# Performance work log

Hardware: AMD Instinct MI355X
Metric: run time of the kernel (lower is better)

Reference implementation:

```python
import jax, jax.numpy as jnp
import numpy as np

B, NSTEP, NSAMPLE = 16, 32, 10
EMBED, STATE, VOCAB, TOTAL = 128, 512, 32000, 8192
STD_SCALE = 0.113
EPS = 1e-5


def setup_inputs() -> dict:
    key = jax.random.key(0)
    ks = jax.random.split(key, 9)
    g = lambda k, shape: jax.random.normal(k, shape, jnp.float32) * 0.05
    return {
        "zi": jax.random.randint(ks[0], (B,), 0, TOTAL),
        "y": jax.random.randint(ks[1], (B, NSTEP), 0, VOCAB),
        "rd": jax.random.uniform(ks[2], (NSTEP, B, NSAMPLE), jnp.float32),
        "latent": g(ks[3], (TOTAL, EMBED)),
        "state_pref_W": g(ks[4], (STATE, 2 * EMBED)),
        "state_pref_b": g(ks[5], (STATE,)),
        "state_move": g(ks[6], (STATE, EMBED)),
        "vocab_W": g(ks[7], (VOCAB, EMBED)),
        "vocab_b": g(ks[8], (VOCAB,)),
    }


def reference(zi, y, rd, latent, state_pref_W, state_pref_b, state_move, vocab_W, vocab_b):
    # z: [B, NSAMPLE, D] -- latent row per batch element, repeated over samples
    z0 = jnp.repeat(latent[zi][:, None, :], NSAMPLE, axis=1)

    def step(carry, rd_t):
        z, zold, lp = carry
        # per-step normalization (torch std is unbiased, ddof=1)
        z = z / (EPS + jnp.std(z, axis=-1, ddof=1, keepdims=True)) * STD_SCALE
        pref = jnp.concatenate([zold, z], axis=-1) @ state_pref_W.T + state_pref_b  # [B,S,STATE]
        xp = jax.nn.softmax(pref, axis=-1)
        xpc = jnp.cumsum(xp, axis=-1)
        # first index where rd < cumulative prob (argmax of bool = first True)
        which = jnp.argmax(rd_t[:, :, None] < xpc, axis=-1)  # [B,S]
        xps = jnp.take_along_axis(xp, which[:, :, None], axis=-1)[..., 0]
        lp = lp + jnp.log(xps)
        mvs = state_move[which]  # [B,S,D]
        return (z + mvs, z, mvs), mvs

    init = (z0, jnp.zeros_like(z0), jnp.zeros((B, NSAMPLE), jnp.float32))
    # note: carry slot 2 of init is lp=0; fix tuple to match step outputs
    init = (z0, jnp.zeros_like(z0), jnp.zeros((B, NSAMPLE), jnp.float32))

    def step_fixed(carry, rd_t):
        z, zold, lp = carry
        z = z / (EPS + jnp.std(z, axis=-1, ddof=1, keepdims=True)) * STD_SCALE
        pref = jnp.concatenate([zold, z], axis=-1) @ state_pref_W.T + state_pref_b
        xp = jax.nn.softmax(pref, axis=-1)
        xpc = jnp.cumsum(xp, axis=-1)
        which = jnp.argmax(rd_t[:, :, None] < xpc, axis=-1)
        xps = jnp.take_along_axis(xp, which[:, :, None], axis=-1)[..., 0]
        lp = lp + jnp.log(xps)
        mvs = state_move[which]
        return (z + mvs, z, lp), mvs

    (_, _, lp), emits = jax.lax.scan(step_fixed, init, rd)  # emits: [T,B,S,D]
    emits = jnp.transpose(emits, (1, 0, 2, 3))  # [B,T,S,D]
    ys = jax.nn.log_softmax(emits @ vocab_W.T + vocab_b, axis=-1)  # [B,T,S,V]
    idx = jnp.broadcast_to(y[:, :, None, None], (B, NSTEP, NSAMPLE, 1))
    yp = jnp.take_along_axis(ys, idx, axis=-1)[..., 0]  # [B,T,S]
    return yp.mean(axis=2)  # [B,T]
```

## Files before the change

### kernel.cpp

```cpp
#include <hip/hip_runtime.h>
#include <hip/hip_bf16.h>

#define B_ 16
#define T_ 32
#define NS_ 10
#define D_ 128
#define ST_ 512
#define V_ 32000
#define NCHAIN 160
#define NLOGZ 250
#define NBLK2 (NCHAIN + NLOGZ)

using short8  = __attribute__((ext_vector_type(8))) short;
using f32x4   = __attribute__((ext_vector_type(4))) float;
using half8   = __attribute__((ext_vector_type(8))) _Float16;
using half2v  = __attribute__((ext_vector_type(2))) _Float16;

__device__ __forceinline__ unsigned short f2bf(float f){
  unsigned u = __float_as_uint(f);
  u += 0x7FFFu + ((u >> 16) & 1u);
  return (unsigned short)(u >> 16);
}
__device__ __forceinline__ unsigned packbf(float a, float b){
  return ((unsigned)f2bf(b) << 16) | (unsigned)f2bf(a);
}
__device__ __forceinline__ unsigned short f2h(float f){
  return __builtin_bit_cast(unsigned short, (_Float16)f);
}
__device__ __forceinline__ float h2f(unsigned u, int hi){
  half2v h = __builtin_bit_cast(half2v, u);
  return (float)h[hi];
}
__device__ __forceinline__ float readlane_f(float v, int lane){
  return __int_as_float(__builtin_amdgcn_readlane(__float_as_int(v), lane));
}

#define DPPADD(x, ctrl, rm) { \
  int _t = __builtin_amdgcn_update_dpp(0, __float_as_int(x), ctrl, rm, 0xf, true); \
  x += __int_as_float(_t); }

__global__ __launch_bounds__(256) void prep_kernel(
    const int* __restrict__ zi, const float* __restrict__ latent,
    const float* __restrict__ prefW, const float* __restrict__ move,
    unsigned short* __restrict__ Hh, unsigned short* __restrict__ Lh,
    unsigned short* __restrict__ Gh,
    float* __restrict__ HU0, float* __restrict__ LU0, float* __restrict__ D0,
    float2* __restrict__ S0, float2* __restrict__ SM,
    unsigned* __restrict__ mbf, float* __restrict__ partial,
    float* __restrict__ out, int* __restrict__ logzdone,
    int* __restrict__ scandone)
{
  const int bid = blockIdx.x, t = threadIdx.x;
  const int lane = t & 63, wv = t >> 6;
  const int c16 = lane & 15, q = lane >> 4;

  if (bid < 192){
    const int sg = bid / 24, tile = bid % 24;
    half8 afr[4][4];
    #pragma unroll
    for (int rt = 0; rt < 4; ++rt){
      const float* mp = move + (sg*64 + rt*16 + c16)*D_ + q*8;
      #pragma unroll
      for (int kk = 0; kk < 4; ++kk){
        float4 f0 = *(const float4*)(mp + kk*32);
        float4 f1 = *(const float4*)(mp + kk*32 + 4);
        half8 a;
        a[0]=(_Float16)f0.x; a[1]=(_Float16)f0.y; a[2]=(_Float16)f0.z; a[3]=(_Float16)f0.w;
        a[4]=(_Float16)f1.x; a[5]=(_Float16)f1.y; a[6]=(_Float16)f1.z; a[7]=(_Float16)f1.w;
        afr[rt][kk] = a;
      }
    }
    const int ct = tile*64 + wv*16 + c16;
    const float* bp; unsigned short* base; int ccol;
    if (ct < 512)      { bp = prefW + ct*256 + 128; base = Hh; ccol = ct; }
    else if (ct < 1024){ bp = prefW + (ct-512)*256; base = Lh; ccol = ct-512; }
    else               { bp = move + (ct-1024)*128; base = Gh; ccol = ct-1024; }
    half8 bfr[4];
    #pragma unroll
    for (int kk = 0; kk < 4; ++kk){
      float4 f0 = *(const float4*)(bp + q*8 + kk*32);
      float4 f1 = *(const float4*)(bp + q*8 + kk*32 + 4);
      half8 bb;
      bb[0]=(_Float16)f0.x; bb[1]=(_Float16)f0.y; bb[2]=(_Float16)f0.z; bb[3]=(_Float16)f0.w;
      bb[4]=(_Float16)f1.x; bb[5]=(_Float16)f1.y; bb[6]=(_Float16)f1.z; bb[7]=(_Float16)f1.w;
      bfr[kk] = bb;
    }
    #pragma unroll
    for (int rt = 0; rt < 4; ++rt){
      f32x4 acc = {0.f,0.f,0.f,0.f};
      #pragma unroll
      for (int kk = 0; kk < 4; ++kk)
        acc = __builtin_amdgcn_mfma_f32_16x16x32_f16(afr[rt][kk], bfr[kk], acc, 0, 0, 0);
      #pragma unroll
      for (int r = 0; r < 4; ++r){
        const int w = sg*64 + rt*16 + q*4 + r;
        base[w*ST_ + ccol] = f2h(acc[r]);
      }
    }
  } else {
    const int b = bid - 192;
    __shared__ float zl[128];
    if (t < 128) zl[t] = latent[zi[b]*D_ + t];
    __syncthreads();

    #pragma unroll
    for (int ii = 0; ii < 2; ++ii){
      const int sidx = t + ii*256;
      const float* wr = prefW + sidx*256;
      const float* mv = move + sidx*128;
      float hu = 0.f, lu = 0.f, d0 = 0.f;
      #pragma unroll 8
      for (int j = 0; j < 128; j += 4){
        float4 w0 = *(const float4*)(wr + j);
        float4 w1 = *(const float4*)(wr + 128 + j);
        float4 m  = *(const float4*)(mv + j);
        float4 z  = *(const float4*)(&zl[j]);
        lu += w0.x*z.x + w0.y*z.y + w0.z*z.z + w0.w*z.w;
        hu += w1.x*z.x + w1.y*z.y + w1.z*z.z + w1.w*z.w;
        d0 += m.x*z.x + m.y*z.y + m.z*z.z + m.w*z.w;
      }
      HU0[b*ST_ + sidx] = hu; LU0[b*ST_ + sidx] = lu; D0[b*ST_ + sidx] = d0;
    }
    if (t < 64){
      float a = zl[t], bb = zl[t + 64];
      float s1 = a + bb, s2 = a*a + bb*bb;
      #pragma unroll
      for (int m = 1; m < 64; m <<= 1){ s1 += __shfl_xor(s1, m, 64); s2 += __shfl_xor(s2, m, 64); }
      if (t == 0) S0[b] = make_float2(s1, s2);
    }
    {
      const int w = b*32 + (t >> 3);
      const float* mw = move + w*128 + (t & 7)*16;
      float4 m0 = *(const float4*)(mw),   m1 = *(const float4*)(mw+4);
      float4 m2 = *(const float4*)(mw+8), m3 = *(const float4*)(mw+12);
      float s1 = m0.x+m0.y+m0.z+m0.w + m1.x+m1.y+m1.z+m1.w
               + m2.x+m2.y+m2.z+m2.w + m3.x+m3.y+m3.z+m3.w;
      float s2 = m0.x*m0.x+m0.y*m0.y+m0.z*m0.z+m0.w*m0.w
               + m1.x*m1.x+m1.y*m1.y+m1.z*m1.z+m1.w*m1.w
               + m2.x*m2.x+m2.y*m2.y+m2.z*m2.z+m2.w*m2.w
               + m3.x*m3.x+m3.y*m3.y+m3.z*m3.z+m3.w*m3.w;
      #pragma unroll
      for (int m = 1; m < 8; m <<= 1){ s1 += __shfl_xor(s1, m, 64); s2 += __shfl_xor(s2, m, 64); }
      if ((t & 7) == 0) SM[w] = make_float2(s1, s2);
      unsigned* dst = mbf + w*64 + (t & 7)*8;
      dst[0] = packbf(m0.x,m0.y); dst[1] = packbf(m0.z,m0.w);
      dst[2] = packbf(m1.x,m1.y); dst[3] = packbf(m1.z,m1.w);
      dst[4] = packbf(m2.x,m2.y); dst[5] = packbf(m2.z,m2.w);
      dst[6] = packbf(m3.x,m3.y); dst[7] = packbf(m3.z,m3.w);
    }
    if (t < 32){ partial[b*32 + t] = 0.f; out[b*32 + t] = 0.f; }
    if (b == 0 && t == 64) *logzdone = 0;
    if (b == 0 && t == 65) *scandone = 0;
  }
}

__global__ __launch_bounds__(256) void workdots_kernel(
    const unsigned short* __restrict__ Hh, const unsigned short* __restrict__ Lh,
    const unsigned short* __restrict__ Gh, const float2* __restrict__ SM,
    const float* __restrict__ HU0, const float* __restrict__ LU0,
    const float* __restrict__ D0, const float2* __restrict__ S0,
    const float* __restrict__ prefB, const float* __restrict__ rd,
    int* __restrict__ whichOut,
    const unsigned* __restrict__ mbf, const float* __restrict__ vw,
    const float* __restrict__ vb, float* __restrict__ partial,
    const int* __restrict__ y, const float* __restrict__ move,
    float* __restrict__ out, int* __restrict__ logzdone,
    int* __restrict__ scandone)
{
  __shared__ float les[2048];
  __shared__ int whichs[T_];
  __shared__ int lastFlag;
  const int bid = blockIdx.x, t = threadIdx.x;
  const int lane = t & 63, wv = t >> 6;
  const int c16 = lane & 15, q = lane >> 4;

  if (bid < NCHAIN){
    if (t < 64){
      const int c = bid, b = c / NS_;
      const int l = t, t0 = l*8;

      float HU[8], LU[8], D[8], prev1[8], bias[8];
      #pragma unroll
      for (int k = 0; k < 8; k += 4){
        float4 h = *(const float4*)(HU0 + b*ST_ + t0 + k);
        float4 u = *(const float4*)(LU0 + b*ST_ + t0 + k);
        float4 d = *(const float4*)(D0  + b*ST_ + t0 + k);
        float4 bb= *(const float4*)(prefB + t0 + k);
        HU[k]=h.x; HU[k+1]=h.y; HU[k+2]=h.z; HU[k+3]=h.w;
        LU[k]=u.x; LU[k+1]=u.y; LU[k+2]=u.z; LU[k+3]=u.w;
        D[k]=d.x;  D[k+1]=d.y;  D[k+2]=d.z;  D[k+3]=d.w;
        bias[k]=bb.x; bias[k+1]=bb.y; bias[k+2]=bb.z; bias[k+3]=bb.w;
      }
      #pragma unroll
      for (int k = 0; k < 8; ++k) prev1[k] = 0.f;
      float2 s0 = S0[b];
      float S1 = s0.x, S2 = s0.y;
      float rdreg = (l < T_) ? rd[l*(B_*NS_) + c] : 0.f;

      for (int st = 0; st < T_; ++st){
        const float mean = S1 * (1.f/128.f);
        const float var  = (S2 - 128.f*mean*mean) * (1.f/127.f);
        const float sc   = 0.113f / (1e-5f + sqrtf(var));

        float cum[8]; float run = 0.f;
        #pragma unroll
        for (int k = 0; k < 8; ++k){
          float pref = fmaf(sc, HU[k], prev1[k] + bias[k]);
          run += __expf(pref);
          cum[k] = run;
        }
        float incl = run;
        DPPADD(incl, 0x111, 0xf)
        DPPADD(incl, 0x112, 0xf)
        DPPADD(incl, 0x114, 0xf)
        DPPADD(incl, 0x118, 0xf)
        DPPADD(incl, 0x142, 0xa)
        DPPADD(incl, 0x143, 0xc)
        const float total  = readlane_f(incl, 63);
        const float target = readlane_f(rdreg, st) * total;

        const bool cond = target < incl;
        const unsigned long long bal = __ballot(cond);
        const float excl = incl - run;
        int kw = 7; float dcand = D[7];
        #pragma unroll
        for (int k = 6; k >= 0; --k){
          bool ck = target < excl + cum[k];
          kw = ck ? k : kw;
          dcand = ck ? D[k] : dcand;
        }
        int which; float dW;
        if (bal){
          const int wlane = __ffsll(bal) - 1;
          which = __builtin_amdgcn_readlane(t0 + kw, wlane);
          dW    = readlane_f(dcand, wlane);
        } else {
          which = 0;
          dW    = readlane_f(D[0], 0);
        }
        if (l == 0){ whichs[st] = which; whichOut[c*T_ + st] = which; }

        const int rb = which*ST_ + t0;
        const uint4 hq = *(const uint4*)(Hh + rb);
        const uint4 lq = *(const uint4*)(Lh + rb);
        const uint4 gq = *(const uint4*)(Gh + rb);
        const float2 sm = SM[which];
        const unsigned ha[4] = {hq.x, hq.y, hq.z, hq.w};
        const unsigned la[4] = {lq.x, lq.y, lq.z, lq.w};
        const unsigned ga[4] = {gq.x, gq.y, gq.z, gq.w};
        #pragma unroll
        for (int k = 0; k < 8; ++k){
          const float Hk = h2f(ha[k>>1], k&1);
          const float Lk = h2f(la[k>>1], k&1);
          const float Gk = h2f(ga[k>>1], k&1);
          const float p1 = sc * LU[k];
          HU[k] = fmaf(sc, HU[k], Hk);
          LU[k] = p1 + Lk;
          D[k]  = fmaf(sc, D[k], Gk);
          prev1[k] = p1;
        }
        S1 = fmaf(sc, S1, sm.x);
        S2 = fmaf(sc*sc, S2, fmaf(2.f*sc, dW, sm.y));
      }
    }
    __syncthreads();

    if (t == 0){
      __threadfence();
      __hip_atomic_fetch_add(scandone, 1, __ATOMIC_RELEASE,
                             __HIP_MEMORY_SCOPE_AGENT);
    }

    {
      const int b = bid / NS_;
      #pragma unroll
      for (int k = 0; k < 8; ++k){
        const int st = wv*8 + k;
        const int w  = whichs[st];
        const int yr = y[b*T_ + st];
        float dot = move[w*D_ + lane]      * vw[yr*D_ + lane]
                  + move[w*D_ + 64 + lane] * vw[yr*D_ + 64 + lane];
        #pragma unroll
        for (int m = 1; m < 64; m <<= 1) dot += __shfl_xor(dot, m, 64);
        if (lane == 0)
          atomicAdd(&out[b*T_ + st], (dot + vb[yr]) * (1.f/NS_));
      }
    }
  } else {
    const int u = bid - NCHAIN;
    const char* mb = (const char*)mbf;
    const int vbase = u*128 + wv*32;
    short8 afr[2][4];
    float vbr[2][4];
    #pragma unroll
    for (int vt = 0; vt < 2; ++vt){
      const int vr = vbase + vt*16 + c16;
      const float* wp = vw + vr*D_ + q*8;
      #pragma unroll
      for (int kk = 0; kk < 4; ++kk){
        float4 f0 = *(const float4*)(wp + kk*32);
        float4 f1 = *(const float4*)(wp + kk*32 + 4);
        short8 a;
        a[0]=(short)f2bf(f0.x); a[1]=(short)f2bf(f0.y);
        a[2]=(short)f2bf(f0.z); a[3]=(short)f2bf(f0.w);
        a[4]=(short)f2bf(f1.x); a[5]=(short)f2bf(f1.y);
        a[6]=(short)f2bf(f1.z); a[7]=(short)f2bf(f1.w);
        afr[vt][kk] = a;
      }
      #pragma unroll
      for (int r = 0; r < 4; ++r)
        vbr[vt][r] = vb[vbase + vt*16 + q*4 + r];
    }

    #pragma unroll 2
    for (int s = 0; s < 32; ++s){
      short8 bfr[4];
      #pragma unroll
      for (int kk = 0; kk < 4; ++kk){
        const int row = s*16 + c16;
        bfr[kk] = *(const short8*)(mb + row*256 + q*16 + kk*64);
      }
      float es = 0.f;
      #pragma unroll
      for (int vt = 0; vt < 2; ++vt){
        f32x4 acc = {0.f,0.f,0.f,0.f};
        #pragma unroll
        for (int kk = 0; kk < 4; ++kk)
          acc = __builtin_amdgcn_mfma_f32_16x16x32_bf16(afr[vt][kk], bfr[kk], acc, 0, 0, 0);
        #pragma unroll
        for (int r = 0; r < 4; ++r)
          es += __expf(acc[r] + vbr[vt][r]);
      }
      es += __shfl_xor(es, 16, 64);
      es += __shfl_xor(es, 32, 64);
      if (lane < 16) les[wv*512 + s*16 + lane] = es;
    }
    __syncthreads();
    #pragma unroll
    for (int i = 0; i < 2; ++i){
      const int st = t + i*256;
      atomicAdd(&partial[st], les[st] + les[512+st] + les[1024+st] + les[1536+st]);
    }
    __syncthreads();

    if (t == 0){
      const int ticket = __hip_atomic_fetch_add(logzdone, 1, __ATOMIC_ACQ_REL,
                                                __HIP_MEMORY_SCOPE_AGENT);
      lastFlag = (ticket == NLOGZ - 1);
    }
    __syncthreads();
    if (lastFlag){
      if (t == 0){
        while (__hip_atomic_load(scandone, __ATOMIC_RELAXED,
                                 __HIP_MEMORY_SCOPE_AGENT) < NCHAIN)
          __builtin_amdgcn_s_sleep(8);
      }
      __syncthreads();
      __builtin_amdgcn_fence(__ATOMIC_ACQUIRE, "agent");
      for (int p = t; p < B_*T_; p += 256){
        const int b = p >> 5, st = p & 31;
        float ls = 0.f;
        #pragma unroll
        for (int s = 0; s < NS_; ++s)
          ls += __logf(partial[whichOut[(b*NS_ + s)*T_ + st]]);
        atomicAdd(&out[b*T_ + st], -ls * (1.f/NS_));
      }
    }
  }
}

extern "C" void kernel_launch(void* const* d_in, const int* in_sizes, int n_in,
                              void* d_out, int out_size, void* d_ws, size_t ws_size,
                              hipStream_t stream)
{
  const int*   zi     = (const int*)d_in[0];
  const int*   y      = (const int*)d_in[1];
  const float* rd     = (const float*)d_in[2];
  const float* latent = (const float*)d_in[3];
  const float* prefW  = (const float*)d_in[4];
  const float* prefB  = (const float*)d_in[5];
  const float* move   = (const float*)d_in[6];
  const float* vw     = (const float*)d_in[7];
  const float* vb     = (const float*)d_in[8];
  float* out = (float*)d_out;

  char* ws = (char*)d_ws;
  unsigned short* Hh = (unsigned short*)(ws);
  unsigned short* Lh = (unsigned short*)(ws + 524288);
  unsigned short* Gh = (unsigned short*)(ws + 1048576);
  float2* SM    = (float2*)(ws + 1572864);
  float*  HU0   = (float*)(ws + 1576960);
  float*  LU0   = (float*)(ws + 1609728);
  float*  D0    = (float*)(ws + 1642496);
  float2* S0    = (float2*)(ws + 1675264);
  float*  partial = (float*)(ws + 1675392);
  int*    which = (int*)(ws + 1677440);
  unsigned* mbf = (unsigned*)(ws + 1697920);
  int*    logzdone = (int*)(ws + 1828992);
  int*    scandone = (int*)(ws + 1828996);

  hipLaunchKernelGGL(prep_kernel, dim3(208), dim3(256), 0, stream,
                     zi, latent, prefW, move, Hh, Lh, Gh,
                     HU0, LU0, D0, S0, SM, mbf, partial, out,
                     logzdone, scandone);
  hipLaunchKernelGGL(workdots_kernel, dim3(NBLK2), dim3(256), 0, stream,
                     Hh, Lh, Gh, SM, HU0, LU0, D0, S0, prefB, rd, which,
                     mbf, vw, vb, partial, y, move, out, logzdone, scandone);
}
```

Baseline: 74.91 us.

## Interleave H/L/G tables per row, prefetch them into L2, stage SM in LDS

Result: faster. 73.08 us (-2.4%).

```diff
diff --git a/kernel.cpp b/kernel.cpp
--- a/kernel.cpp
+++ b/kernel.cpp
@@ -13,6 +13,7 @@
 
 using short8  = __attribute__((ext_vector_type(8))) short;
 using f32x4   = __attribute__((ext_vector_type(4))) float;
+using fvec4   = __attribute__((ext_vector_type(4))) float;
 using half8   = __attribute__((ext_vector_type(8))) _Float16;
 using half2v  = __attribute__((ext_vector_type(2))) _Float16;
 
@@ -39,11 +40,11 @@
   int _t = __builtin_amdgcn_update_dpp(0, __float_as_int(x), ctrl, rm, 0xf, true); \
   x += __int_as_float(_t); }
 
+
 __global__ __launch_bounds__(256) void prep_kernel(
     const int* __restrict__ zi, const float* __restrict__ latent,
     const float* __restrict__ prefW, const float* __restrict__ move,
-    unsigned short* __restrict__ Hh, unsigned short* __restrict__ Lh,
-    unsigned short* __restrict__ Gh,
+    unsigned short* __restrict__ fused,
     float* __restrict__ HU0, float* __restrict__ LU0, float* __restrict__ D0,
     float2* __restrict__ S0, float2* __restrict__ SM,
     unsigned* __restrict__ mbf, float* __restrict__ partial,
@@ -71,10 +72,10 @@
       }
     }
     const int ct = tile*64 + wv*16 + c16;
-    const float* bp; unsigned short* base; int ccol;
-    if (ct < 512)      { bp = prefW + ct*256 + 128; base = Hh; ccol = ct; }
-    else if (ct < 1024){ bp = prefW + (ct-512)*256; base = Lh; ccol = ct-512; }
-    else               { bp = move + (ct-1024)*128; base = Gh; ccol = ct-1024; }
+    const float* bp; int sect, ccol;
+    if (ct < 512)      { bp = prefW + ct*256 + 128; sect = 0; ccol = ct; }
+    else if (ct < 1024){ bp = prefW + (ct-512)*256; sect = 1; ccol = ct-512; }
+    else               { bp = move + (ct-1024)*128; sect = 2; ccol = ct-1024; }
     half8 bfr[4];
     #pragma unroll
     for (int kk = 0; kk < 4; ++kk){
@@ -85,6 +86,7 @@
       bb[4]=(_Float16)f1.x; bb[5]=(_Float16)f1.y; bb[6]=(_Float16)f1.z; bb[7]=(_Float16)f1.w;
       bfr[kk] = bb;
     }
+    const int foff = ((ccol >> 3) << 5) + sect*8 + (ccol & 7);
     #pragma unroll
     for (int rt = 0; rt < 4; ++rt){
       f32x4 acc = {0.f,0.f,0.f,0.f};
@@ -94,7 +96,7 @@
       #pragma unroll
       for (int r = 0; r < 4; ++r){
         const int w = sg*64 + rt*16 + q*4 + r;
-        base[w*ST_ + ccol] = f2h(acc[r]);
+        fused[w*2048 + foff] = f2h(acc[r]);
       }
     }
   } else {
@@ -155,8 +157,7 @@
 }
 
 __global__ __launch_bounds__(256) void workdots_kernel(
-    const unsigned short* __restrict__ Hh, const unsigned short* __restrict__ Lh,
-    const unsigned short* __restrict__ Gh, const float2* __restrict__ SM,
+    const unsigned short* __restrict__ fused, const float2* __restrict__ SMg,
     const float* __restrict__ HU0, const float* __restrict__ LU0,
     const float* __restrict__ D0, const float2* __restrict__ S0,
     const float* __restrict__ prefB, const float* __restrict__ rd,
@@ -168,6 +169,7 @@
     int* __restrict__ scandone)
 {
   __shared__ float les[2048];
+  __shared__ float2 sml[ST_];
   __shared__ int whichs[T_];
   __shared__ int lastFlag;
   const int bid = blockIdx.x, t = threadIdx.x;
@@ -175,6 +177,12 @@
   const int c16 = lane & 15, q = lane >> 4;
 
   if (bid < NCHAIN){
+    if (wv == 1){
+      #pragma unroll
+      for (int j = 0; j < 8; ++j) sml[(t - 64)*8 + j] = SMg[(t - 64)*8 + j];
+    }
+    __syncthreads();
+
     if (t < 64){
       const int c = bid, b = c / NS_;
       const int l = t, t0 = l*8;
@@ -197,6 +205,7 @@
       float S1 = s0.x, S2 = s0.y;
       float rdreg = (l < T_) ? rd[l*(B_*NS_) + c] : 0.f;
 
+      __builtin_amdgcn_s_setprio(1);
       for (int st = 0; st < T_; ++st){
         const float mean = S1 * (1.f/128.f);
         const float var  = (S2 - 128.f*mean*mean) * (1.f/127.f);
@@ -240,11 +249,11 @@
         }
         if (l == 0){ whichs[st] = which; whichOut[c*T_ + st] = which; }
 
-        const int rb = which*ST_ + t0;
-        const uint4 hq = *(const uint4*)(Hh + rb);
-        const uint4 lq = *(const uint4*)(Lh + rb);
-        const uint4 gq = *(const uint4*)(Gh + rb);
-        const float2 sm = SM[which];
+        const char* fp = (const char*)fused + ((unsigned)which << 12) + (unsigned)(l << 6);
+        const uint4 hq = *(const uint4*)(fp);
+        const uint4 lq = *(const uint4*)(fp + 16);
+        const uint4 gq = *(const uint4*)(fp + 32);
+        const float2 sm = sml[which];
         const unsigned ha[4] = {hq.x, hq.y, hq.z, hq.w};
         const unsigned la[4] = {lq.x, lq.y, lq.z, lq.w};
         const unsigned ga[4] = {gq.x, gq.y, gq.z, gq.w};
@@ -262,6 +271,20 @@
         S1 = fmaf(sc, S1, sm.x);
         S2 = fmaf(sc*sc, S2, fmaf(2.f*sc, dW, sm.y));
       }
+      __builtin_amdgcn_s_setprio(0);
+    } else {
+      const float* fb = (const float*)fused;
+      const int slice = bid >> 3;
+      const int r0 = slice*26;
+      const int r1 = (r0 + 26 < 512) ? (r0 + 26) : 512;
+      float acc = 0.f;
+      for (int r = r0; r < r1; ++r){
+        for (int off = (t - 64)*4; off < 1024; off += 192*4){
+          fvec4 v = *(const fvec4*)(fb + (unsigned)r*1024 + off);
+          acc += v[0] + v[1] + v[2] + v[3];
+        }
+      }
+      asm volatile("" :: "v"(acc));
     }
     __syncthreads();
 
@@ -298,13 +321,13 @@
       const float* wp = vw + vr*D_ + q*8;
       #pragma unroll
       for (int kk = 0; kk < 4; ++kk){
-        float4 f0 = *(const float4*)(wp + kk*32);
-        float4 f1 = *(const float4*)(wp + kk*32 + 4);
+        fvec4 f0 = __builtin_nontemporal_load((const fvec4*)(wp + kk*32));
+        fvec4 f1 = __builtin_nontemporal_load((const fvec4*)(wp + kk*32 + 4));
         short8 a;
-        a[0]=(short)f2bf(f0.x); a[1]=(short)f2bf(f0.y);
-        a[2]=(short)f2bf(f0.z); a[3]=(short)f2bf(f0.w);
-        a[4]=(short)f2bf(f1.x); a[5]=(short)f2bf(f1.y);
-        a[6]=(short)f2bf(f1.z); a[7]=(short)f2bf(f1.w);
+        a[0]=(short)f2bf(f0[0]); a[1]=(short)f2bf(f0[1]);
+        a[2]=(short)f2bf(f0[2]); a[3]=(short)f2bf(f0[3]);
+        a[4]=(short)f2bf(f1[0]); a[5]=(short)f2bf(f1[1]);
+        a[6]=(short)f2bf(f1[2]); a[7]=(short)f2bf(f1[3]);
         afr[vt][kk] = a;
       }
       #pragma unroll
@@ -385,25 +408,23 @@
   float* out = (float*)d_out;
 
   char* ws = (char*)d_ws;
-  unsigned short* Hh = (unsigned short*)(ws);
-  unsigned short* Lh = (unsigned short*)(ws + 524288);
-  unsigned short* Gh = (unsigned short*)(ws + 1048576);
-  float2* SM    = (float2*)(ws + 1572864);
-  float*  HU0   = (float*)(ws + 1576960);
-  float*  LU0   = (float*)(ws + 1609728);
-  float*  D0    = (float*)(ws + 1642496);
-  float2* S0    = (float2*)(ws + 1675264);
-  float*  partial = (float*)(ws + 1675392);
-  int*    which = (int*)(ws + 1677440);
-  unsigned* mbf = (unsigned*)(ws + 1697920);
-  int*    logzdone = (int*)(ws + 1828992);
-  int*    scandone = (int*)(ws + 1828996);
+  unsigned short* fused = (unsigned short*)(ws);
+  float2* SM    = (float2*)(ws + 2097152);
+  float*  HU0   = (float*)(ws + 2101248);
+  float*  LU0   = (float*)(ws + 2134016);
+  float*  D0    = (float*)(ws + 2166784);
+  float2* S0    = (float2*)(ws + 2199552);
+  float*  partial = (float*)(ws + 2199680);
+  int*    which = (int*)(ws + 2201728);
+  unsigned* mbf = (unsigned*)(ws + 2222208);
+  int*    logzdone = (int*)(ws + 2353280);
+  int*    scandone = (int*)(ws + 2353284);
 
   hipLaunchKernelGGL(prep_kernel, dim3(208), dim3(256), 0, stream,
-                     zi, latent, prefW, move, Hh, Lh, Gh,
+                     zi, latent, prefW, move, fused,
                      HU0, LU0, D0, S0, SM, mbf, partial, out,
                      logzdone, scandone);
   hipLaunchKernelGGL(workdots_kernel, dim3(NBLK2), dim3(256), 0, stream,
-                     Hh, Lh, Gh, SM, HU0, LU0, D0, S0, prefB, rd, which,
+                     fused, SM, HU0, LU0, D0, S0, prefB, rd, which,
                      mbf, vw, vb, partial, y, move, out, logzdone, scandone);
 }
```
